# Optimization experiments

Hardware: AMD Instinct MI355X
Metric: run time of the kernel (lower is better)

Reference implementation:

```python
import jax, jax.numpy as jnp
import numpy as np

ROPE_BASE = 10000.0


def _rope_cos_sin(n, d, dtype):
    # standard llama-style rotary embedding over head dim d
    inv_freq = 1.0 / (ROPE_BASE ** (jnp.arange(0, d, 2, dtype=jnp.float32) / d))
    t = jnp.arange(n, dtype=jnp.float32)
    freqs = jnp.einsum('n,f->nf', t, inv_freq)          # [N, d/2]
    emb = jnp.concatenate([freqs, freqs], axis=-1)      # [N, d]
    return jnp.cos(emb).astype(dtype), jnp.sin(emb).astype(dtype)


def _rotate_half(x):
    x1, x2 = jnp.split(x, 2, axis=-1)
    return jnp.concatenate([-x2, x1], axis=-1)


def _apply_rope(x, cos, sin):
    # x: [B, H, N, D]; cos/sin: [N, D] broadcast over B, H
    return x * cos + _rotate_half(x) * sin


def setup_inputs() -> dict:
    key = jax.random.key(0)
    k1, k2, k3 = jax.random.split(key, 3)
    B, N, dim = 2, 2048, 1024
    heads, dim_head = 16, 64
    inner = heads * dim_head
    x = jax.random.normal(k1, (B, N, dim), dtype=jnp.float32)
    w_qkv = jax.random.normal(k2, (dim, 3 * inner), dtype=jnp.float32) * (dim ** -0.5)
    w_out = jax.random.normal(k3, (inner, dim), dtype=jnp.float32) * (inner ** -0.5)
    return {"x": x, "w_qkv": w_qkv, "w_out": w_out}


def reference(x, w_qkv, w_out):
    B, N, _ = x.shape
    heads, dim_head = 16, 64
    qkv = jnp.einsum('bnd,de->bne', x, w_qkv)
    q, k, v = jnp.split(qkv, 3, axis=-1)
    def to_heads(t):
        return t.reshape(B, N, heads, dim_head).transpose(0, 2, 1, 3)  # [B,H,N,D]
    q, k, v = to_heads(q), to_heads(k), to_heads(v)
    cos, sin = _rope_cos_sin(N, dim_head, x.dtype)
    q = _apply_rope(q, cos, sin)
    k = _apply_rope(k, cos, sin)
    scale = dim_head ** -0.5
    scores = jnp.einsum('bhqd,bhkd->bhqk', q, k) * scale   # [B,H,N,N], non-causal
    attn = jax.nn.softmax(scores, axis=-1)
    out = jnp.einsum('bhqk,bhkd->bhqd', attn, v)
    out = out.transpose(0, 2, 1, 3).reshape(B, N, heads * dim_head)
    return jnp.einsum('bne,ed->bnd', out, w_out)
```

## Files before the change

### kernel.cpp

```cpp
#include <hip/hip_runtime.h>

typedef __attribute__((ext_vector_type(8))) short bf16x8;
typedef __attribute__((ext_vector_type(4))) float f32x4;

#define MFMA(a, b, c) __builtin_amdgcn_mfma_f32_16x16x32_bf16(a, b, c, 0, 0, 0)

__device__ __forceinline__ unsigned short f2bf(float f) {
    unsigned u = __builtin_bit_cast(unsigned, f);
    u += 0x7fffu + ((u >> 16) & 1u);
    return (unsigned short)(u >> 16);
}

__device__ __forceinline__ void gload16(const unsigned short* g, unsigned short* l) {
    __builtin_amdgcn_global_load_lds(
        (const __attribute__((address_space(1))) void*)g,
        (__attribute__((address_space(3))) void*)l, 16, 0, 0);
}

__device__ __forceinline__ unsigned pack_bf16(float lo, float hi) {
    unsigned a = __builtin_bit_cast(unsigned, lo) + 0x8000u;
    unsigned b = __builtin_bit_cast(unsigned, hi) + 0x8000u;
    return __builtin_amdgcn_perm(b, a, 0x07060302);
}


__global__ __launch_bounds__(256) void cvt_bf16(const float* __restrict__ in,
                                                unsigned short* __restrict__ out, int n) {
    int i = (blockIdx.x * 256 + threadIdx.x) * 4;
    if (i < n) {
        float4 f = *(const float4*)(in + i);
        ushort4 u;
        u.x = f2bf(f.x); u.y = f2bf(f.y); u.z = f2bf(f.z); u.w = f2bf(f.w);
        *(ushort4*)(out + i) = u;
    }
}

__global__ __launch_bounds__(256) void transpose_cvt(const float* __restrict__ in,
                                                     unsigned short* __restrict__ out,
                                                     int R, int C) {
    __shared__ float tile[32][33];
    const int c0 = blockIdx.x * 32, r0 = blockIdx.y * 32;
    const int tr = threadIdx.x >> 3;
    const int j4 = (threadIdx.x & 7) * 4;
    float4 f = *(const float4*)(in + (size_t)(r0 + tr) * C + c0 + j4);
    tile[tr][j4 + 0] = f.x; tile[tr][j4 + 1] = f.y;
    tile[tr][j4 + 2] = f.z; tile[tr][j4 + 3] = f.w;
    __syncthreads();
    ushort4 u;
    u.x = f2bf(tile[j4 + 0][tr]); u.y = f2bf(tile[j4 + 1][tr]);
    u.z = f2bf(tile[j4 + 2][tr]); u.w = f2bf(tile[j4 + 3][tr]);
    *(ushort4*)(out + (size_t)(c0 + tr) * R + r0 + j4) = u;
}

__global__ __launch_bounds__(256) void rope_tab(float* __restrict__ cosT,
                                                float* __restrict__ sinT) {
    int i = blockIdx.x * 256 + threadIdx.x;
    int n = i >> 5, f = i & 31;
    float ang = (float)n * exp2f((float)f * -0.4152410118609203f);
    float s, c;
    sincosf(ang, &s, &c);
    cosT[i] = c; sinT[i] = s;
}


template <int EPI>
__global__ __launch_bounds__(256, 3) void gemm_bt(const unsigned short* __restrict__ A,
                                                  const unsigned short* __restrict__ Bt,
                                                  int K, int Ncols,
                                                  unsigned short* __restrict__ oq,
                                                  unsigned short* __restrict__ ok,
                                                  unsigned short* __restrict__ ovt,
                                                  float* __restrict__ of,
                                                  const float* __restrict__ cosT,
                                                  const float* __restrict__ sinT) {
    __shared__ unsigned short As[2][128 * 32];
    __shared__ unsigned short Bs[2][128 * 32];
    const int tid = threadIdx.x;
    const int w = tid >> 6, lane = tid & 63, quad = lane >> 4, cc = lane & 15;
    const int wm = w >> 1, wn = w & 1;
    const int m0 = blockIdx.y * 128, n0 = blockIdx.x * 128;

    size_t aoff[2], boff[2];
#pragma unroll
    for (int t = 0; t < 2; t++) {
        int S = w * 128 + t * 64 + lane;
        int row = S >> 2;
        int c = (S & 3) ^ ((row >> 1) & 3);
        aoff[t] = (size_t)(m0 + row) * K + c * 8;
        boff[t] = (size_t)(n0 + row) * K + c * 8;
    }

#pragma unroll
    for (int t = 0; t < 2; t++) {
        gload16(A + aoff[t], &As[0][(w * 2 + t) * 512]);
        gload16(Bt + boff[t], &Bs[0][(w * 2 + t) * 512]);
    }
    __syncthreads();

    f32x4 acc[4][4] = {};
    const int rpos = (quad ^ ((cc >> 1) & 3)) * 8;
    const int nkt = K >> 5;

    for (int kt = 0; kt < nkt; kt++) {
        const int pb = kt & 1;
        if (kt < nkt - 1) {
            const int ko = (kt + 1) * 32;
#pragma unroll
            for (int t = 0; t < 2; t++) {
                gload16(A + aoff[t] + ko, &As[pb ^ 1][(w * 2 + t) * 512]);
                gload16(Bt + boff[t] + ko, &Bs[pb ^ 1][(w * 2 + t) * 512]);
            }
        }
        bf16x8 af[4], bf[4];
#pragma unroll
        for (int i = 0; i < 4; i++)
            af[i] = *(const bf16x8*)&As[pb][(wm * 64 + i * 16 + cc) * 32 + rpos];
#pragma unroll
        for (int i = 0; i < 4; i++)
            bf[i] = *(const bf16x8*)&Bs[pb][(wn * 64 + i * 16 + cc) * 32 + rpos];
#pragma unroll
        for (int i = 0; i < 4; i++)
#pragma unroll
            for (int j = 0; j < 4; j++)
                acc[i][j] = MFMA(af[i], bf[j], acc[i][j]);
        __syncthreads();
    }

    if (EPI == 0) {
        const int e0 = n0 + wn * 64;
        const int which = e0 >> 10;
        const int h = (e0 >> 6) & 15;
        if (which < 2) {
            unsigned short* dst = (which == 0) ? oq : ok;
            const float postscale = (which == 0) ? 0.125f : 1.0f;
#pragma unroll
            for (int mf = 0; mf < 4; mf++) {
#pragma unroll
                for (int r = 0; r < 4; r++) {
                    int mg = m0 + wm * 64 + mf * 16 + quad * 4 + r;
                    int nseq = mg & 2047, b = mg >> 11;
                    float vals[4];
#pragma unroll
                    for (int nf = 0; nf < 4; nf++) vals[nf] = acc[mf][nf][r];
                    size_t rowbase = ((size_t)(b * 16 + h) * 2048 + nseq) * 64;
#pragma unroll
                    for (int nf = 0; nf < 4; nf++) {
                        int d = nf * 16 + cc;
                        int f = d & 31;
                        float cs = cosT[nseq * 32 + f];
                        float sn = sinT[nseq * 32 + f];
                        float partner = vals[nf ^ 2];
                        float outv = (vals[nf] * cs +
                                      ((nf < 2) ? -partner : partner) * sn) * postscale;
                        dst[rowbase + d] = f2bf(outv);
                    }
                }
            }
        } else {
#pragma unroll
            for (int mf = 0; mf < 4; mf++) {
                int mg0 = m0 + wm * 64 + mf * 16 + quad * 4;
                int b = mg0 >> 11, nseq = mg0 & 2047;
#pragma unroll
                for (int nf = 0; nf < 4; nf++) {
                    int d = nf * 16 + cc;
                    ushort4 pk;
                    pk.x = f2bf(acc[mf][nf][0]);
                    pk.y = f2bf(acc[mf][nf][1]);
                    pk.z = f2bf(acc[mf][nf][2]);
                    pk.w = f2bf(acc[mf][nf][3]);
                    *(ushort4*)(ovt + ((size_t)(b * 16 + h) * 64 + d) * 2048 + nseq) = pk;
                }
            }
        }
    } else {
#pragma unroll
        for (int mf = 0; mf < 4; mf++)
#pragma unroll
            for (int nf = 0; nf < 4; nf++)
#pragma unroll
                for (int r = 0; r < 4; r++) {
                    int mg = m0 + wm * 64 + mf * 16 + quad * 4 + r;
                    of[(size_t)mg * Ncols + n0 + wn * 64 + nf * 16 + cc] = acc[mf][nf][r];
                }
    }
}


__global__ __launch_bounds__(256, 2) void attn(const unsigned short* __restrict__ q,
                                               const unsigned short* __restrict__ k,
                                               const unsigned short* __restrict__ vt,
                                               unsigned short* __restrict__ o) {
    __shared__ unsigned short ks[2][64 * 64];
    __shared__ unsigned short vs[2][64 * 64];
    __shared__ unsigned short ps[128 * 72];
    __shared__ float rsb[128];
    const int tid = threadIdx.x;
    const int w = tid >> 6, lane = tid & 63, quad = lane >> 4, cc = lane & 15;
    const int bh = blockIdx.x & 31, qt = blockIdx.x >> 5;

    const unsigned short* qg = q + ((size_t)bh * 2048 + qt * 128 + w * 32) * 64;
    bf16x8 aq[2][2];
#pragma unroll
    for (int mf = 0; mf < 2; mf++)
#pragma unroll
        for (int kc = 0; kc < 2; kc++)
            aq[mf][kc] = *(const bf16x8*)(qg + (mf * 16 + cc) * 64 + kc * 32 + quad * 8);

    int koff[2], voff[2];
#pragma unroll
    for (int t = 0; t < 2; t++) {
        int S = w * 128 + t * 64 + lane;
        int row = S >> 3;
        int c = (S & 7) ^ (row & 7);
        koff[t] = row * 64 + c * 8;
        voff[t] = row * 2048 + c * 8;
    }

    const unsigned short* kg0 = k + (size_t)bh * 2048 * 64;
    const unsigned short* vg0 = vt + (size_t)bh * 64 * 2048;

#pragma unroll
    for (int t = 0; t < 2; t++) {
        gload16(kg0 + koff[t], &ks[0][(w * 2 + t) * 512]);
        gload16(vg0 + voff[t], &vs[0][(w * 2 + t) * 512]);
    }
    __syncthreads();

    f32x4 oacc[2][4] = {};
    float rs[2] = {};

    for (int kt = 0; kt < 32; kt++) {
        const int pb = kt & 1;
        if (kt < 31) {
            const unsigned short* kb = kg0 + (kt + 1) * 4096;
            const unsigned short* vb = vg0 + (kt + 1) * 64;
#pragma unroll
            for (int t = 0; t < 2; t++) {
                gload16(kb + koff[t], &ks[pb ^ 1][(w * 2 + t) * 512]);
                gload16(vb + voff[t], &vs[pb ^ 1][(w * 2 + t) * 512]);
            }
        }

        f32x4 s2[2][4] = {};
#pragma unroll
        for (int kc = 0; kc < 2; kc++) {
#pragma unroll
            for (int nf = 0; nf < 4; nf++) {
                bf16x8 bk = *(const bf16x8*)&ks[pb][(nf * 16 + cc) * 64 +
                                                    ((kc * 4 + quad) ^ (cc & 7)) * 8];
                s2[0][nf] = MFMA(bk, aq[0][kc], s2[0][nf]);
                s2[1][nf] = MFMA(bk, aq[1][kc], s2[1][nf]);
            }
        }

#pragma unroll
        for (int mf = 0; mf < 2; mf++) {
#pragma unroll
            for (int nf = 0; nf < 4; nf++) {
                float p0 = __builtin_amdgcn_exp2f(
                    __builtin_fmaf(s2[mf][nf][0], 1.44269504f, -11.54156036f));
                float p1 = __builtin_amdgcn_exp2f(
                    __builtin_fmaf(s2[mf][nf][1], 1.44269504f, -11.54156036f));
                float p2 = __builtin_amdgcn_exp2f(
                    __builtin_fmaf(s2[mf][nf][2], 1.44269504f, -11.54156036f));
                float p3 = __builtin_amdgcn_exp2f(
                    __builtin_fmaf(s2[mf][nf][3], 1.44269504f, -11.54156036f));
                rs[mf] += (p0 + p1) + (p2 + p3);
                uint2 pk;
                pk.x = pack_bf16(p0, p1);
                pk.y = pack_bf16(p2, p3);
                *(uint2*)&ps[(w * 32 + mf * 16 + cc) * 72 + nf * 16 + quad * 4] = pk;
            }
        }

#pragma unroll
        for (int kc = 0; kc < 2; kc++) {
            bf16x8 ap[2];
            ap[0] = *(const bf16x8*)&ps[(w * 32 + cc) * 72 + kc * 32 + quad * 8];
            ap[1] = *(const bf16x8*)&ps[(w * 32 + 16 + cc) * 72 + kc * 32 + quad * 8];
#pragma unroll
            for (int df = 0; df < 4; df++) {
                bf16x8 bv = *(const bf16x8*)&vs[pb][(df * 16 + cc) * 64 +
                                                    ((kc * 4 + quad) ^ (cc & 7)) * 8];
                oacc[0][df] = MFMA(ap[0], bv, oacc[0][df]);
                oacc[1][df] = MFMA(ap[1], bv, oacc[1][df]);
            }
        }

        __syncthreads();
    }

#pragma unroll
    for (int mf = 0; mf < 2; mf++) {
        rs[mf] += __shfl_xor(rs[mf], 16, 64);
        rs[mf] += __shfl_xor(rs[mf], 32, 64);
    }
    if (quad == 0) {
        rsb[w * 32 + cc] = rs[0];
        rsb[w * 32 + 16 + cc] = rs[1];
    }

#pragma unroll
    for (int mf = 0; mf < 2; mf++) {
        f32x4 rv = *(const f32x4*)&rsb[w * 32 + mf * 16 + quad * 4];
        f32x4 inv;
#pragma unroll
        for (int r = 0; r < 4; r++) inv[r] = 1.0f / rv[r];
#pragma unroll
        for (int r = 0; r < 4; r++)
#pragma unroll
            for (int df = 0; df < 4; df++)
                ps[(w * 32 + mf * 16 + quad * 4 + r) * 72 + df * 16 + cc] =
                    f2bf(oacc[mf][df][r] * inv[r]);
    }
    __syncthreads();
    {
        const int b = bh >> 4, h = bh & 15;
        int row = tid >> 1, hf = tid & 1;
        unsigned short* og =
            o + ((size_t)(b * 2048 + qt * 128 + row)) * 1024 + h * 64 + hf * 32;
#pragma unroll
        for (int j = 0; j < 4; j++)
            *(uint4*)(og + j * 8) = *(const uint4*)&ps[row * 72 + hf * 32 + j * 8];
    }
}


extern "C" void kernel_launch(void* const* d_in, const int* in_sizes, int n_in,
                              void* d_out, int out_size, void* d_ws, size_t ws_size,
                              hipStream_t stream) {
    const float* x = (const float*)d_in[0];
    const float* w_qkv = (const float*)d_in[1];
    const float* w_out = (const float*)d_in[2];
    float* out = (float*)d_out;

    unsigned short* xb    = (unsigned short*)d_ws;
    unsigned short* wqkvT = xb + 4096 * 1024;
    unsigned short* woutT = wqkvT + 3072 * 1024;
    unsigned short* qb    = woutT + 1024 * 1024;
    unsigned short* kb    = qb + 2 * 16 * 2048 * 64;
    unsigned short* vtb   = kb + 2 * 16 * 2048 * 64;
    unsigned short* ob    = vtb + 2 * 16 * 2048 * 64;
    float* cosT = (float*)(ob + 4096 * 1024);
    float* sinT = cosT + 2048 * 32;

    rope_tab<<<256, 256, 0, stream>>>(cosT, sinT);
    cvt_bf16<<<4096, 256, 0, stream>>>(x, xb, 4096 * 1024);
    transpose_cvt<<<dim3(96, 32), 256, 0, stream>>>(w_qkv, wqkvT, 1024, 3072);
    transpose_cvt<<<dim3(32, 32), 256, 0, stream>>>(w_out, woutT, 1024, 1024);
    gemm_bt<0><<<dim3(24, 32), 256, 0, stream>>>(xb, wqkvT, 1024, 3072,
                                                 qb, kb, vtb, nullptr, cosT, sinT);
    attn<<<512, 256, 0, stream>>>(qb, kb, vtb, ob);
    gemm_bt<1><<<dim3(8, 32), 256, 0, stream>>>(ob, woutT, 1024, 1024,
                                                nullptr, nullptr, nullptr, out,
                                                nullptr, nullptr);
}
```

Before: 190.2 us.

## Split attention work across 8 waves of 16 rows and add MFMA priority hints

The attention kernel now launches 512 threads per block, so each of 8 waves handles 16 query rows instead of 4 waves handling 32. Each wave now issues one K/V tile load per iteration instead of two, and register use per wave roughly halves, which should allow more waves resident per CU. s_setprio hints are wrapped around the MFMA sections so matrix work gets scheduling priority. In exchange, each K/V LDS fragment is read by twice as many waves, and every block-wide barrier now has to synchronise 8 waves.

```diff
diff --git a/kernel.cpp b/kernel.cpp
--- a/kernel.cpp
+++ b/kernel.cpp
@@ -187,7 +187,7 @@
 }
 
 
-__global__ __launch_bounds__(256, 2) void attn(const unsigned short* __restrict__ q,
+__global__ __launch_bounds__(512, 4) void attn(const unsigned short* __restrict__ q,
                                                const unsigned short* __restrict__ k,
                                                const unsigned short* __restrict__ vt,
                                                unsigned short* __restrict__ o) {
@@ -199,111 +199,89 @@
     const int w = tid >> 6, lane = tid & 63, quad = lane >> 4, cc = lane & 15;
     const int bh = blockIdx.x & 31, qt = blockIdx.x >> 5;
 
-    const unsigned short* qg = q + ((size_t)bh * 2048 + qt * 128 + w * 32) * 64;
-    bf16x8 aq[2][2];
-#pragma unroll
-    for (int mf = 0; mf < 2; mf++)
-#pragma unroll
-        for (int kc = 0; kc < 2; kc++)
-            aq[mf][kc] = *(const bf16x8*)(qg + (mf * 16 + cc) * 64 + kc * 32 + quad * 8);
-
-    int koff[2], voff[2];
-#pragma unroll
-    for (int t = 0; t < 2; t++) {
-        int S = w * 128 + t * 64 + lane;
-        int row = S >> 3;
-        int c = (S & 7) ^ (row & 7);
-        koff[t] = row * 64 + c * 8;
-        voff[t] = row * 2048 + c * 8;
-    }
+    const unsigned short* qg = q + ((size_t)bh * 2048 + qt * 128 + w * 16) * 64;
+    bf16x8 aq[2];
+#pragma unroll
+    for (int kc = 0; kc < 2; kc++)
+        aq[kc] = *(const bf16x8*)(qg + cc * 64 + kc * 32 + quad * 8);
+
+    const int S = w * 64 + lane;
+    const int row = S >> 3;
+    const int c = (S & 7) ^ (row & 7);
+    const int koff = row * 64 + c * 8;
+    const int voff = row * 2048 + c * 8;
 
     const unsigned short* kg0 = k + (size_t)bh * 2048 * 64;
     const unsigned short* vg0 = vt + (size_t)bh * 64 * 2048;
 
-#pragma unroll
-    for (int t = 0; t < 2; t++) {
-        gload16(kg0 + koff[t], &ks[0][(w * 2 + t) * 512]);
-        gload16(vg0 + voff[t], &vs[0][(w * 2 + t) * 512]);
-    }
+    gload16(kg0 + koff, &ks[0][w * 512]);
+    gload16(vg0 + voff, &vs[0][w * 512]);
     __syncthreads();
 
-    f32x4 oacc[2][4] = {};
-    float rs[2] = {};
+    f32x4 oacc[4] = {};
+    float rs = 0.f;
 
     for (int kt = 0; kt < 32; kt++) {
         const int pb = kt & 1;
         if (kt < 31) {
             const unsigned short* kb = kg0 + (kt + 1) * 4096;
             const unsigned short* vb = vg0 + (kt + 1) * 64;
-#pragma unroll
-            for (int t = 0; t < 2; t++) {
-                gload16(kb + koff[t], &ks[pb ^ 1][(w * 2 + t) * 512]);
-                gload16(vb + voff[t], &vs[pb ^ 1][(w * 2 + t) * 512]);
-            }
-        }
-
-        f32x4 s2[2][4] = {};
+            gload16(kb + koff, &ks[pb ^ 1][w * 512]);
+            gload16(vb + voff, &vs[pb ^ 1][w * 512]);
+        }
+
+        f32x4 s2[4] = {};
+        __builtin_amdgcn_s_setprio(1);
 #pragma unroll
         for (int kc = 0; kc < 2; kc++) {
 #pragma unroll
             for (int nf = 0; nf < 4; nf++) {
                 bf16x8 bk = *(const bf16x8*)&ks[pb][(nf * 16 + cc) * 64 +
                                                     ((kc * 4 + quad) ^ (cc & 7)) * 8];
-                s2[0][nf] = MFMA(bk, aq[0][kc], s2[0][nf]);
-                s2[1][nf] = MFMA(bk, aq[1][kc], s2[1][nf]);
-            }
-        }
-
-#pragma unroll
-        for (int mf = 0; mf < 2; mf++) {
-#pragma unroll
-            for (int nf = 0; nf < 4; nf++) {
-                float p0 = __builtin_amdgcn_exp2f(
-                    __builtin_fmaf(s2[mf][nf][0], 1.44269504f, -11.54156036f));
-                float p1 = __builtin_amdgcn_exp2f(
-                    __builtin_fmaf(s2[mf][nf][1], 1.44269504f, -11.54156036f));
-                float p2 = __builtin_amdgcn_exp2f(
-                    __builtin_fmaf(s2[mf][nf][2], 1.44269504f, -11.54156036f));
-                float p3 = __builtin_amdgcn_exp2f(
-                    __builtin_fmaf(s2[mf][nf][3], 1.44269504f, -11.54156036f));
-                rs[mf] += (p0 + p1) + (p2 + p3);
-                uint2 pk;
-                pk.x = pack_bf16(p0, p1);
-                pk.y = pack_bf16(p2, p3);
-                *(uint2*)&ps[(w * 32 + mf * 16 + cc) * 72 + nf * 16 + quad * 4] = pk;
-            }
+                s2[nf] = MFMA(bk, aq[kc], s2[nf]);
+            }
+        }
+        __builtin_amdgcn_s_setprio(0);
+
+#pragma unroll
+        for (int nf = 0; nf < 4; nf++) {
+            float p0 = __builtin_amdgcn_exp2f(
+                __builtin_fmaf(s2[nf][0], 1.44269504f, -11.54156036f));
+            float p1 = __builtin_amdgcn_exp2f(
+                __builtin_fmaf(s2[nf][1], 1.44269504f, -11.54156036f));
+            float p2 = __builtin_amdgcn_exp2f(
+                __builtin_fmaf(s2[nf][2], 1.44269504f, -11.54156036f));
+            float p3 = __builtin_amdgcn_exp2f(
+                __builtin_fmaf(s2[nf][3], 1.44269504f, -11.54156036f));
+            rs += (p0 + p1) + (p2 + p3);
+            uint2 pk;
+            pk.x = pack_bf16(p0, p1);
+            pk.y = pack_bf16(p2, p3);
+            *(uint2*)&ps[(w * 16 + cc) * 72 + nf * 16 + quad * 4] = pk;
         }
 
 #pragma unroll
         for (int kc = 0; kc < 2; kc++) {
-            bf16x8 ap[2];
-            ap[0] = *(const bf16x8*)&ps[(w * 32 + cc) * 72 + kc * 32 + quad * 8];
-            ap[1] = *(const bf16x8*)&ps[(w * 32 + 16 + cc) * 72 + kc * 32 + quad * 8];
+            bf16x8 ap = *(const bf16x8*)&ps[(w * 16 + cc) * 72 + kc * 32 + quad * 8];
+            __builtin_amdgcn_s_setprio(1);
 #pragma unroll
             for (int df = 0; df < 4; df++) {
                 bf16x8 bv = *(const bf16x8*)&vs[pb][(df * 16 + cc) * 64 +
                                                     ((kc * 4 + quad) ^ (cc & 7)) * 8];
-                oacc[0][df] = MFMA(ap[0], bv, oacc[0][df]);
-                oacc[1][df] = MFMA(ap[1], bv, oacc[1][df]);
-            }
+                oacc[df] = MFMA(ap, bv, oacc[df]);
+            }
+            __builtin_amdgcn_s_setprio(0);
         }
 
         __syncthreads();
     }
 
-#pragma unroll
-    for (int mf = 0; mf < 2; mf++) {
-        rs[mf] += __shfl_xor(rs[mf], 16, 64);
-        rs[mf] += __shfl_xor(rs[mf], 32, 64);
-    }
-    if (quad == 0) {
-        rsb[w * 32 + cc] = rs[0];
-        rsb[w * 32 + 16 + cc] = rs[1];
-    }
-
-#pragma unroll
-    for (int mf = 0; mf < 2; mf++) {
-        f32x4 rv = *(const f32x4*)&rsb[w * 32 + mf * 16 + quad * 4];
+    rs += __shfl_xor(rs, 16, 64);
+    rs += __shfl_xor(rs, 32, 64);
+    if (quad == 0) rsb[w * 16 + cc] = rs;
+
+    {
+        f32x4 rv = *(const f32x4*)&rsb[w * 16 + quad * 4];
         f32x4 inv;
 #pragma unroll
         for (int r = 0; r < 4; r++) inv[r] = 1.0f / rv[r];
@@ -311,18 +289,18 @@
         for (int r = 0; r < 4; r++)
 #pragma unroll
             for (int df = 0; df < 4; df++)
-                ps[(w * 32 + mf * 16 + quad * 4 + r) * 72 + df * 16 + cc] =
-                    f2bf(oacc[mf][df][r] * inv[r]);
+                ps[(w * 16 + quad * 4 + r) * 72 + df * 16 + cc] =
+                    f2bf(oacc[df][r] * inv[r]);
     }
     __syncthreads();
     {
         const int b = bh >> 4, h = bh & 15;
-        int row = tid >> 1, hf = tid & 1;
+        int row2 = tid >> 2, seg = tid & 3;
         unsigned short* og =
-            o + ((size_t)(b * 2048 + qt * 128 + row)) * 1024 + h * 64 + hf * 32;
-#pragma unroll
-        for (int j = 0; j < 4; j++)
-            *(uint4*)(og + j * 8) = *(const uint4*)&ps[row * 72 + hf * 32 + j * 8];
+            o + ((size_t)(b * 2048 + qt * 128 + row2)) * 1024 + h * 64 + seg * 16;
+#pragma unroll
+        for (int j = 0; j < 2; j++)
+            *(uint4*)(og + j * 8) = *(const uint4*)&ps[row2 * 72 + seg * 16 + j * 8];
     }
 }
 
@@ -351,7 +329,7 @@
     transpose_cvt<<<dim3(32, 32), 256, 0, stream>>>(w_out, woutT, 1024, 1024);
     gemm_bt<0><<<dim3(24, 32), 256, 0, stream>>>(xb, wqkvT, 1024, 3072,
                                                  qb, kb, vtb, nullptr, cosT, sinT);
-    attn<<<512, 256, 0, stream>>>(qb, kb, vtb, ob);
+    attn<<<512, 512, 0, stream>>>(qb, kb, vtb, ob);
     gemm_bt<1><<<dim3(8, 32), 256, 0, stream>>>(ob, woutT, 1024, 1024,
                                                 nullptr, nullptr, nullptr, out,
                                                 nullptr, nullptr);
```

Measured after the change: 186.0 us. 2.2% less time.

## Split attention KV range across two wave groups and keep P in registers

Applied to the files above, without the earlier changes.

The attention kernel goes from 256 to 512 threads per block. Two wave groups each process half of the key/value sequence for the same query rows, and their partial outputs and row sums are combined through LDS at the end. The softmax probabilities are no longer staged through shared memory: permlane swap instructions rearrange them in registers into the MFMA A-operand layout. s_setprio is also raised around the MFMA sections. The aim is more waves in flight to hide latency and fewer LDS round trips, at the cost of a final reduction step, a larger LDS footprint and direct scalar bf16 global stores.

```diff
diff --git a/kernel.cpp b/kernel.cpp
--- a/kernel.cpp
+++ b/kernel.cpp
@@ -187,19 +187,18 @@
 }
 
 
-__global__ __launch_bounds__(256, 2) void attn(const unsigned short* __restrict__ q,
+__global__ __launch_bounds__(512, 4) void attn(const unsigned short* __restrict__ q,
                                                const unsigned short* __restrict__ k,
                                                const unsigned short* __restrict__ vt,
                                                unsigned short* __restrict__ o) {
-    __shared__ unsigned short ks[2][64 * 64];
-    __shared__ unsigned short vs[2][64 * 64];
-    __shared__ unsigned short ps[128 * 72];
-    __shared__ float rsb[128];
+    __shared__ unsigned short kvbuf[2][2][2][64 * 64];
+    __shared__ float rsr[2][128];
     const int tid = threadIdx.x;
     const int w = tid >> 6, lane = tid & 63, quad = lane >> 4, cc = lane & 15;
+    const int g = w & 1, s = w >> 1;
     const int bh = blockIdx.x & 31, qt = blockIdx.x >> 5;
 
-    const unsigned short* qg = q + ((size_t)bh * 2048 + qt * 128 + w * 32) * 64;
+    const unsigned short* qg = q + ((size_t)bh * 2048 + qt * 128 + s * 32) * 64;
     bf16x8 aq[2][2];
 #pragma unroll
     for (int mf = 0; mf < 2; mf++)
@@ -207,55 +206,58 @@
         for (int kc = 0; kc < 2; kc++)
             aq[mf][kc] = *(const bf16x8*)(qg + (mf * 16 + cc) * 64 + kc * 32 + quad * 8);
 
-    int koff[2], voff[2];
+    int koff[2], voff[2], ldso[2];
 #pragma unroll
     for (int t = 0; t < 2; t++) {
-        int S = w * 128 + t * 64 + lane;
-        int row = S >> 3;
-        int c = (S & 7) ^ (row & 7);
+        int S2 = (s * 2 + t) * 64 + lane;
+        int row = S2 >> 3;
+        int c = (S2 & 7) ^ (row & 7);
         koff[t] = row * 64 + c * 8;
         voff[t] = row * 2048 + c * 8;
-    }
-
-    const unsigned short* kg0 = k + (size_t)bh * 2048 * 64;
-    const unsigned short* vg0 = vt + (size_t)bh * 64 * 2048;
+        ldso[t] = (s * 2 + t) * 512;
+    }
+
+    const unsigned short* kgg = k + (size_t)bh * 2048 * 64 + (size_t)g * 16 * 4096;
+    const unsigned short* vgg = vt + (size_t)bh * 64 * 2048 + (size_t)g * 16 * 64;
 
 #pragma unroll
     for (int t = 0; t < 2; t++) {
-        gload16(kg0 + koff[t], &ks[0][(w * 2 + t) * 512]);
-        gload16(vg0 + voff[t], &vs[0][(w * 2 + t) * 512]);
+        gload16(kgg + koff[t], &kvbuf[0][g][0][ldso[t]]);
+        gload16(vgg + voff[t], &kvbuf[1][g][0][ldso[t]]);
     }
     __syncthreads();
 
     f32x4 oacc[2][4] = {};
     float rs[2] = {};
 
-    for (int kt = 0; kt < 32; kt++) {
-        const int pb = kt & 1;
-        if (kt < 31) {
-            const unsigned short* kb = kg0 + (kt + 1) * 4096;
-            const unsigned short* vb = vg0 + (kt + 1) * 64;
+    for (int i = 0; i < 16; i++) {
+        const int pb = i & 1;
+        if (i < 15) {
 #pragma unroll
             for (int t = 0; t < 2; t++) {
-                gload16(kb + koff[t], &ks[pb ^ 1][(w * 2 + t) * 512]);
-                gload16(vb + voff[t], &vs[pb ^ 1][(w * 2 + t) * 512]);
-            }
-        }
-
+                gload16(kgg + (i + 1) * 4096 + koff[t], &kvbuf[0][g][pb ^ 1][ldso[t]]);
+                gload16(vgg + (i + 1) * 64 + voff[t], &kvbuf[1][g][pb ^ 1][ldso[t]]);
+            }
+        }
+
+        const unsigned short* kb = &kvbuf[0][g][pb][0];
         f32x4 s2[2][4] = {};
-#pragma unroll
-        for (int kc = 0; kc < 2; kc++) {
+        __builtin_amdgcn_s_setprio(1);
+#pragma unroll
+        for (int kc = 0; kc < 2; kc++)
 #pragma unroll
             for (int nf = 0; nf < 4; nf++) {
-                bf16x8 bk = *(const bf16x8*)&ks[pb][(nf * 16 + cc) * 64 +
-                                                    ((kc * 4 + quad) ^ (cc & 7)) * 8];
+                bf16x8 bk = *(const bf16x8*)&kb[(nf * 16 + cc) * 64 +
+                                                ((kc * 4 + quad) ^ (cc & 7)) * 8];
                 s2[0][nf] = MFMA(bk, aq[0][kc], s2[0][nf]);
                 s2[1][nf] = MFMA(bk, aq[1][kc], s2[1][nf]);
             }
-        }
-
+        __builtin_amdgcn_s_setprio(0);
+
+        bf16x8 ap[2][2];
 #pragma unroll
         for (int mf = 0; mf < 2; mf++) {
+            unsigned X[4][2];
 #pragma unroll
             for (int nf = 0; nf < 4; nf++) {
                 float p0 = __builtin_amdgcn_exp2f(
@@ -267,26 +269,35 @@
                 float p3 = __builtin_amdgcn_exp2f(
                     __builtin_fmaf(s2[mf][nf][3], 1.44269504f, -11.54156036f));
                 rs[mf] += (p0 + p1) + (p2 + p3);
-                uint2 pk;
-                pk.x = pack_bf16(p0, p1);
-                pk.y = pack_bf16(p2, p3);
-                *(uint2*)&ps[(w * 32 + mf * 16 + cc) * 72 + nf * 16 + quad * 4] = pk;
-            }
-        }
-
-#pragma unroll
-        for (int kc = 0; kc < 2; kc++) {
-            bf16x8 ap[2];
-            ap[0] = *(const bf16x8*)&ps[(w * 32 + cc) * 72 + kc * 32 + quad * 8];
-            ap[1] = *(const bf16x8*)&ps[(w * 32 + 16 + cc) * 72 + kc * 32 + quad * 8];
+                X[nf][0] = pack_bf16(p0, p1);
+                X[nf][1] = pack_bf16(p2, p3);
+            }
+#pragma unroll
+            for (int kc = 0; kc < 2; kc++) {
+                unsigned a0 = X[kc * 2][0], b0 = X[kc * 2 + 1][0];
+                unsigned a1 = X[kc * 2][1], b1 = X[kc * 2 + 1][1];
+                asm("v_permlane32_swap_b32 %0, %1" : "+v"(a0), "+v"(b0));
+                asm("v_permlane16_swap_b32 %0, %1" : "+v"(a0), "+v"(b0));
+                asm("v_permlane32_swap_b32 %0, %1" : "+v"(a1), "+v"(b1));
+                asm("v_permlane16_swap_b32 %0, %1" : "+v"(a1), "+v"(b1));
+                uint4 dd;
+                dd.x = a0; dd.y = a1; dd.z = b0; dd.w = b1;
+                ap[mf][kc] = __builtin_bit_cast(bf16x8, dd);
+            }
+        }
+
+        const unsigned short* vb = &kvbuf[1][g][pb][0];
+        __builtin_amdgcn_s_setprio(1);
+#pragma unroll
+        for (int kc = 0; kc < 2; kc++)
 #pragma unroll
             for (int df = 0; df < 4; df++) {
-                bf16x8 bv = *(const bf16x8*)&vs[pb][(df * 16 + cc) * 64 +
-                                                    ((kc * 4 + quad) ^ (cc & 7)) * 8];
-                oacc[0][df] = MFMA(ap[0], bv, oacc[0][df]);
-                oacc[1][df] = MFMA(ap[1], bv, oacc[1][df]);
-            }
-        }
+                bf16x8 bv = *(const bf16x8*)&vb[(df * 16 + cc) * 64 +
+                                                ((kc * 4 + quad) ^ (cc & 7)) * 8];
+                oacc[0][df] = MFMA(ap[0][kc], bv, oacc[0][df]);
+                oacc[1][df] = MFMA(ap[1][kc], bv, oacc[1][df]);
+            }
+        __builtin_amdgcn_s_setprio(0);
 
         __syncthreads();
     }
@@ -295,34 +306,43 @@
     for (int mf = 0; mf < 2; mf++) {
         rs[mf] += __shfl_xor(rs[mf], 16, 64);
         rs[mf] += __shfl_xor(rs[mf], 32, 64);
-    }
-    if (quad == 0) {
-        rsb[w * 32 + cc] = rs[0];
-        rsb[w * 32 + 16 + cc] = rs[1];
-    }
-
-#pragma unroll
-    for (int mf = 0; mf < 2; mf++) {
-        f32x4 rv = *(const f32x4*)&rsb[w * 32 + mf * 16 + quad * 4];
-        f32x4 inv;
-#pragma unroll
-        for (int r = 0; r < 4; r++) inv[r] = 1.0f / rv[r];
-#pragma unroll
-        for (int r = 0; r < 4; r++)
+        if (quad == 0) rsr[g][s * 32 + mf * 16 + cc] = rs[mf];
+    }
+
+    float* po = (float*)&kvbuf[0][0][0][0];
+    if (g == 1) {
+#pragma unroll
+        for (int mf = 0; mf < 2; mf++)
 #pragma unroll
             for (int df = 0; df < 4; df++)
-                ps[(w * 32 + mf * 16 + quad * 4 + r) * 72 + df * 16 + cc] =
-                    f2bf(oacc[mf][df][r] * inv[r]);
+#pragma unroll
+                for (int r = 0; r < 4; r++)
+                    po[(s * 32 + mf * 16 + quad * 4 + r) * 68 + df * 16 + cc] =
+                        oacc[mf][df][r];
     }
     __syncthreads();
-    {
+
+    if (g == 0) {
         const int b = bh >> 4, h = bh & 15;
-        int row = tid >> 1, hf = tid & 1;
-        unsigned short* og =
-            o + ((size_t)(b * 2048 + qt * 128 + row)) * 1024 + h * 64 + hf * 32;
-#pragma unroll
-        for (int j = 0; j < 4; j++)
-            *(uint4*)(og + j * 8) = *(const uint4*)&ps[row * 72 + hf * 32 + j * 8];
+#pragma unroll
+        for (int mf = 0; mf < 2; mf++) {
+            const int rbase = s * 32 + mf * 16 + quad * 4;
+            float inv[4];
+#pragma unroll
+            for (int r = 0; r < 4; r++)
+                inv[r] = 1.0f / (rsr[0][rbase + r] + rsr[1][rbase + r]);
+#pragma unroll
+            for (int r = 0; r < 4; r++) {
+                const int grow = qt * 128 + rbase + r;
+                unsigned short* og = o + ((size_t)(b * 2048 + grow)) * 1024 + h * 64;
+#pragma unroll
+                for (int df = 0; df < 4; df++) {
+                    float v = (oacc[mf][df][r] + po[(rbase + r) * 68 + df * 16 + cc]) *
+                              inv[r];
+                    og[df * 16 + cc] = f2bf(v);
+                }
+            }
+        }
     }
 }
 
@@ -351,7 +371,7 @@
     transpose_cvt<<<dim3(32, 32), 256, 0, stream>>>(w_out, woutT, 1024, 1024);
     gemm_bt<0><<<dim3(24, 32), 256, 0, stream>>>(xb, wqkvT, 1024, 3072,
                                                  qb, kb, vtb, nullptr, cosT, sinT);
-    attn<<<512, 256, 0, stream>>>(qb, kb, vtb, ob);
+    attn<<<512, 512, 0, stream>>>(qb, kb, vtb, ob);
     gemm_bt<1><<<dim3(8, 32), 256, 0, stream>>>(ob, woutT, 1024, 1024,
                                                 nullptr, nullptr, nullptr, out,
                                                 nullptr, nullptr);
```

Measured after the change: 192.3 us. About the same (+1.1%).
